# Kernel tuning notes

Hardware: AMD Instinct MI355X
Metric: run time of the kernel (lower is better)

The kernel has to match this reference:

```python
import jax, jax.numpy as jnp
import numpy as np

N, C, V, T = 256, 256, 25, 20
K = 3            # kernel_size
PAD = 1          # padding
O = 256          # out_channels
C4 = C // 4
EPS = 1e-5


def _bn(x, p, axes_shape):
    # p: (4, dim) = gamma, beta, running_mean, running_var (eval-mode BN)
    g, b, m, v = (p[i].reshape(axes_shape) for i in range(4))
    return (x - m) * (g / jnp.sqrt(v + EPS)) + b


def setup_inputs() -> dict:
    key = jax.random.key(0)
    ks = jax.random.split(key, 12)
    rn = lambda k, s, sc=0.05: jax.random.normal(k, s, jnp.float32) * sc
    bn = lambda k, d: jnp.stack([
        1.0 + 0.1 * jax.random.normal(jax.random.fold_in(k, 0), (d,), jnp.float32),  # gamma
        0.1 * jax.random.normal(jax.random.fold_in(k, 1), (d,), jnp.float32),        # beta
        0.1 * jax.random.normal(jax.random.fold_in(k, 2), (d,), jnp.float32),        # mean
        0.5 + jax.random.uniform(jax.random.fold_in(k, 3), (d,), jnp.float32),       # var
    ])
    return {
        "x": jax.random.normal(ks[0], (N, C, V, T), jnp.float32),
        "Wg1": rn(ks[1], (2 * T, T), 0.2),      # Linear T -> 2T (no bias)
        "Wg2": rn(ks[2], (K, 2 * T), 0.2),      # Linear 2T -> K (no bias)
        "Wl1": rn(ks[3], (C4, C, K)),           # Conv1d C -> C/4, kernel K
        "Wl2": rn(ks[4], (C, C4)),              # Conv1d C/4 -> C, kernel 1
        "Wc2": rn(ks[5], (O, C)),               # 1x1 Conv2d C -> O (no bias)
        "bng": bn(ks[6], 2 * T),
        "bnl": bn(ks[7], C4),
        "bn1p": bn(ks[8], C),
        "bn2p": bn(ks[9], O),
    }


def reference(x, Wg1, Wg2, Wl1, Wl2, Wc2, bng, bnl, bn1p, bn2p):
    n, c, v, t = x.shape
    new_x = jnp.transpose(x, (0, 1, 3, 2))            # (N, C, T, V)
    pooled = new_x.mean(axis=-1)                       # (N, C, T)  adaptive_avg_pool over V

    # --- G branch: per-(n,c) dynamic temporal kernel ---
    h = pooled.reshape(n * c, t) @ Wg1.T               # (NC, 2T)
    h = jax.nn.relu(_bn(h, bng, (1, 2 * t)))
    kern = jax.nn.softmax(h @ Wg2.T, axis=-1)          # (NC, K)
    kern = kern.reshape(n, c, K)

    # --- L branch: local temporal excitation ---
    l = jax.lax.conv_general_dilated(
        pooled, Wl1, window_strides=(1,), padding=[(K // 2, K // 2)],
        dimension_numbers=("NCH", "OIH", "NCH"))      # (N, C4, T)
    l = jax.nn.relu(_bn(l, bnl, (1, C4, 1)))
    l = jax.nn.sigmoid(jnp.einsum("oc,nct->not", Wl2, l))  # (N, C, T)
    new_x = new_x + l[..., None]                       # (N, C, T, V)

    # --- dynamic depthwise temporal conv (groups = N*C) ---
    padded = jnp.pad(new_x, ((0, 0), (0, 0), (PAD, PAD), (0, 0)))
    out = sum(kern[:, :, k, None, None] * padded[:, :, k:k + t, :] for k in range(K))

    out = jnp.transpose(out, (0, 1, 3, 2))             # (N, C, V, T)
    out = jax.nn.relu(_bn(out, bn1p, (1, c, 1, 1)))    # bn1 + relu; dropout in eval = identity
    out = jnp.einsum("oc,ncvt->novt", Wc2, out)        # 1x1 conv
    out = jax.nn.relu(_bn(out, bn2p, (1, O, 1, 1)))    # bn2 + relu
    return out
```

## Files before the change

kernel.cpp:

```cpp
#include <hip/hip_runtime.h>
#include <hip/hip_bf16.h>
#include <math.h>

#define N_ 256
#define C_ 256
#define V_ 25
#define T_ 20
#define C4_ 64
#define O_ 256
#define VT_ 500
#define EPS_ 1e-5f

typedef unsigned short ushort_t;
typedef unsigned short us4 __attribute__((ext_vector_type(4)));
typedef short short8 __attribute__((ext_vector_type(8)));
typedef float f32x4 __attribute__((ext_vector_type(4)));

__device__ __forceinline__ float bf2f(ushort_t u) {
    unsigned int v = ((unsigned int)u) << 16;
    return __builtin_bit_cast(float, v);
}
__device__ __forceinline__ ushort_t f2bf(float f) {
    unsigned int u = __builtin_bit_cast(unsigned int, f);
    unsigned int r = u + 0x7fffu + ((u >> 16) & 1u);
    return (ushort_t)(r >> 16);
}

__device__ __forceinline__ void bar_lds() {
    __builtin_amdgcn_sched_barrier(0);
    asm volatile("s_waitcnt lgkmcnt(0)" ::: "memory");
    __builtin_amdgcn_s_barrier();
    __builtin_amdgcn_sched_barrier(0);
}

__global__ __launch_bounds__(256) void k_pool(const float* __restrict__ x,
                                              float* __restrict__ pooled,
                                              const float* __restrict__ Wc2,
                                              ushort_t* __restrict__ wbf,
                                              const float* __restrict__ Wl1,
                                              ushort_t* __restrict__ awl,
                                              const float* __restrict__ Wl2,
                                              ushort_t* __restrict__ wl2bf) {
    int tid = threadIdx.x;
    if (blockIdx.x >= 8272) {
        int o = (blockIdx.x - 8272) * 256 + tid;
        int c4 = o / 768;
        int rem = o - c4 * 768;
        int k = rem >> 8, c = rem & 255;
        awl[o] = f2bf(Wl1[(c4 * 256 + c) * 3 + k]);
        return;
    }
    if (blockIdx.x >= 8256) {
        int i = (blockIdx.x - 8256) * 256 + tid;
        f32x4 v = ((const f32x4*)Wl2)[i];
        us4 o; o.x = f2bf(v.x); o.y = f2bf(v.y); o.z = f2bf(v.z); o.w = f2bf(v.w);
        ((us4*)wl2bf)[i] = o;
        return;
    }
    if (blockIdx.x >= 8192) {
        int i = (blockIdx.x - 8192) * 256 + tid;
        f32x4 v = ((const f32x4*)Wc2)[i];
        us4 o; o.x = f2bf(v.x); o.y = f2bf(v.y); o.z = f2bf(v.z); o.w = f2bf(v.w);
        ((us4*)wbf)[i] = o;
        return;
    }
    __shared__ float xs[8][504];
    const f32x4* src = (const f32x4*)(x + (size_t)blockIdx.x * 8 * VT_);
    for (int i = tid; i < 1000; i += 256) {
        int r = i / 125, cidx = (i % 125) * 4;
        *(f32x4*)&xs[r][cidx] = src[i];
    }
    __syncthreads();
    if (tid < 160) {
        int r = tid / 20, t = tid % 20;
        float s = 0.f;
#pragma unroll
        for (int v = 0; v < V_; ++v) s += xs[r][v * T_ + t];
        pooled[blockIdx.x * 160 + tid] = s * 0.04f;
    }
}

__global__ __launch_bounds__(256) void k_gl(const float* __restrict__ pooled,
                                            const float* __restrict__ Wg1,
                                            const float* __restrict__ Wg2,
                                            const float* __restrict__ bng,
                                            const float* __restrict__ bnl,
                                            const ushort_t* __restrict__ awl,
                                            const ushort_t* __restrict__ wl2bf,
                                            float* __restrict__ kern,
                                            float* __restrict__ l2out) {
    __shared__ __align__(16) char smem[76288];
    float (*pp)[22] = (float (*)[22])smem;
    float* sl = (float*)(smem + 22528);
    float* bl = (float*)(smem + 22528 + 256);
    char* lsT = smem + 23040;
    char* bpt = smem + 27136;

    int tid = threadIdx.x;
    int n = blockIdx.x;

    {
        const f32x4* pn = (const f32x4*)(pooled + n * (C_ * T_));
#pragma unroll
        for (int q = 0; q < 5; ++q) {
            int id = q * 256 + tid;
            int c = id / 5, qq = id % 5;
            f32x4 v = pn[id];
            pp[c][qq * 4 + 0] = v.x; pp[c][qq * 4 + 1] = v.y;
            pp[c][qq * 4 + 2] = v.z; pp[c][qq * 4 + 3] = v.w;
        }
    }
    if (tid < C4_) {
        float g = bnl[tid], b = bnl[64 + tid];
        float m = bnl[128 + tid], v = bnl[192 + tid];
        float s = g * rsqrtf(v + EPS_);
        sl[tid] = s; bl[tid] = b - m * s;
    }
    {
        unsigned int* z = (unsigned int*)lsT;
        for (int i = tid; i < 384; i += 256) z[640 + i] = 0u;
    }
    __syncthreads();

    float p[20];
#pragma unroll
    for (int t = 0; t < 20; ++t) p[t] = pp[tid][t];

    {
        float l0 = 0.f, l1 = 0.f, l2 = 0.f;
#pragma unroll 4
        for (int j = 0; j < 40; ++j) {
            float h = 0.f;
#pragma unroll
            for (int t = 0; t < 20; ++t) h = fmaf(Wg1[j * 20 + t], p[t], h);
            float g = bng[j], b = bng[40 + j];
            float m = bng[80 + j], v = bng[120 + j];
            float s = g * rsqrtf(v + EPS_);
            h = fmaxf(fmaf(h, s, b - m * s), 0.f);
            l0 = fmaf(Wg2[j], h, l0);
            l1 = fmaf(Wg2[40 + j], h, l1);
            l2 = fmaf(Wg2[80 + j], h, l2);
        }
        float mx = fmaxf(l0, fmaxf(l1, l2));
        float e0 = __expf(l0 - mx), e1 = __expf(l1 - mx), e2 = __expf(l2 - mx);
        float inv = 1.f / (e0 + e1 + e2);
        float* kp = kern + (n * C_ + tid) * 3;
        kp[0] = e0 * inv; kp[1] = e1 * inv; kp[2] = e2 * inv;
    }

    {
        int c = tid;
#pragma unroll
        for (int k = 0; k < 3; ++k) {
            int col2base = (k * 256 + c) * 2;
#pragma unroll
            for (int t = 0; t < 20; ++t) {
                int i = t + k - 1;
                float v = (i >= 0 && i < 20) ? p[i] : 0.f;
                int byte = t * 1536 + (col2base ^ ((t & 7) << 4));
                *(ushort_t*)(bpt + byte) = f2bf(v);
            }
        }
    }
    __syncthreads();

    int lane = tid & 63, wave = tid >> 6;
    int mrow = lane & 15, kof = (lane >> 4) * 8, prow = (lane >> 4) * 4;

    {
        f32x4 acc0 = (f32x4){0.f, 0.f, 0.f, 0.f};
        f32x4 acc1 = (f32x4){0.f, 0.f, 0.f, 0.f};
        int swz = ((mrow & 7) << 4);
#pragma unroll 4
        for (int kk = 0; kk < 768; kk += 32) {
            short8 af = *(const short8*)(awl + (wave * 16 + mrow) * 768 + kk + kof);
            short8 b0 = *(const short8*)(bpt + mrow * 1536 + (((kk + kof) * 2) ^ swz));
            short8 b1 = *(const short8*)(bpt + (16 + mrow) * 1536 + (((kk + kof) * 2) ^ swz));
            acc0 = __builtin_amdgcn_mfma_f32_16x16x32_bf16(af, b0, acc0, 0, 0, 0);
            acc1 = __builtin_amdgcn_mfma_f32_16x16x32_bf16(af, b1, acc1, 0, 0, 0);
        }
        f32x4 sv = *(const f32x4*)(sl + wave * 16 + prow);
        f32x4 bv = *(const f32x4*)(bl + wave * 16 + prow);
#pragma unroll
        for (int nt = 0; nt < 2; ++nt) {
            int t = nt * 16 + (lane & 15);
            if (t < 20) {
                f32x4 a = nt ? acc1 : acc0;
#pragma unroll
                for (int r = 0; r < 4; ++r) {
                    int c4 = wave * 16 + prow + r;
                    float v = fmaxf(fmaf(a[r], sv[r], bv[r]), 0.f);
                    int byte = t * 128 + ((c4 * 2) ^ ((t & 7) << 4));
                    *(ushort_t*)(lsT + byte) = f2bf(v);
                }
            }
        }
    }
    __syncthreads();

    {
        f32x4 acc[4][2];
#pragma unroll
        for (int mtl = 0; mtl < 4; ++mtl)
#pragma unroll
            for (int nt = 0; nt < 2; ++nt) acc[mtl][nt] = (f32x4){0.f, 0.f, 0.f, 0.f};
        int swz = ((mrow & 7) << 4);
#pragma unroll
        for (int kk = 0; kk < 64; kk += 32) {
            short8 af[4], bfr[2];
#pragma unroll
            for (int mtl = 0; mtl < 4; ++mtl)
                af[mtl] = *(const short8*)(wl2bf + (wave * 64 + mtl * 16 + mrow) * 64 + kk + kof);
#pragma unroll
            for (int nt = 0; nt < 2; ++nt)
                bfr[nt] = *(const short8*)(lsT + (nt * 16 + mrow) * 128 + (((kk + kof) * 2) ^ swz));
#pragma unroll
            for (int mtl = 0; mtl < 4; ++mtl)
#pragma unroll
                for (int nt = 0; nt < 2; ++nt)
                    acc[mtl][nt] = __builtin_amdgcn_mfma_f32_16x16x32_bf16(af[mtl], bfr[nt], acc[mtl][nt], 0, 0, 0);
        }
#pragma unroll
        for (int nt = 0; nt < 2; ++nt) {
            int t = nt * 16 + (lane & 15);
            if (t < 20) {
#pragma unroll
                for (int mtl = 0; mtl < 4; ++mtl) {
#pragma unroll
                    for (int r = 0; r < 4; ++r) {
                        int c = wave * 64 + mtl * 16 + prow + r;
                        float v = acc[mtl][nt][r];
                        l2out[(n * C_ + c) * T_ + t] = 1.f / (1.f + __expf(-v));
                    }
                }
            }
        }
    }
}

#define YSTRIDE 264

template <int NT>
__device__ __forceinline__ void gemm_pass(const ushort_t* __restrict__ yT,
                                          const ushort_t* __restrict__ wbf,
                                          float* __restrict__ outn,
                                          const int (&ctb)[NT], int ov_idx,
                                          int obase, int mrow, int kof, int prow,
                                          float s2, float b2) {
    f32x4 acc[4][NT];
#pragma unroll
    for (int mt = 0; mt < 4; ++mt)
#pragma unroll
        for (int j = 0; j < NT; ++j) acc[mt][j] = (f32x4){0.f, 0.f, 0.f, 0.f};

#pragma unroll 1
    for (int kk = 0; kk < C_; kk += 32) {
        short8 af[4];
        short8 bfr[NT];
#pragma unroll
        for (int mt = 0; mt < 4; ++mt)
            af[mt] = *(const short8*)(wbf + (obase + mt * 16 + mrow) * C_ + kk + kof);
#pragma unroll
        for (int j = 0; j < NT; ++j)
            bfr[j] = *(const short8*)(yT + (ctb[j] + mrow) * YSTRIDE + kk + kof);
#pragma unroll
        for (int mt = 0; mt < 4; ++mt)
#pragma unroll
            for (int j = 0; j < NT; ++j)
                acc[mt][j] = __builtin_amdgcn_mfma_f32_16x16x32_bf16(af[mt], bfr[j], acc[mt][j], 0, 0, 0);
    }

#pragma unroll
    for (int mt = 0; mt < 4; ++mt) {
#pragma unroll
        for (int r = 0; r < 4; ++r) {
            int lsrc = mt * 16 + prow + r;
            float s2w = __shfl(s2, lsrc);
            float b2w = __shfl(b2, lsrc);
            float* orow = outn + (size_t)(obase + lsrc) * VT_;
#pragma unroll
            for (int j = 0; j < NT; ++j) {
                bool skip = (j == ov_idx) && (mrow < 12);
                if (!skip) {
                    float vr = fmaxf(fmaf(acc[mt][j][r], s2w, b2w), 0.f);
                    orow[ctb[j] + mrow] = vr;
                }
            }
        }
    }
}

__global__ __launch_bounds__(256, 3) void k_main(const float* __restrict__ x,
                                                 const ushort_t* __restrict__ wbf,
                                                 const float* __restrict__ bn1p,
                                                 const float* __restrict__ bn2p,
                                                 const float* __restrict__ kern,
                                                 const float* __restrict__ l2g,
                                                 float* __restrict__ out) {
    __shared__ __align__(16) ushort_t yT[100 * YSTRIDE];

    int tid = threadIdx.x;
    int n = blockIdx.y;
    int vblk = blockIdx.x;
    const float* xn = x + (size_t)n * (C_ * V_ * T_) + vblk * 100;

    float s1, b1, k0, k1, k2, s2, b2, l2r[20];
    {
        int c = tid;
        float g1 = bn1p[c], be1 = bn1p[256 + c];
        float m1 = bn1p[512 + c], v1 = bn1p[768 + c];
        s1 = g1 * rsqrtf(v1 + EPS_);
        b1 = be1 - m1 * s1;
        float g2 = bn2p[c], be2 = bn2p[256 + c];
        float m2 = bn2p[512 + c], v2 = bn2p[768 + c];
        s2 = g2 * rsqrtf(v2 + EPS_);
        b2 = be2 - m2 * s2;
        const float* kp = kern + (n * C_ + c) * 3;
        k0 = kp[0]; k1 = kp[1]; k2 = kp[2];
        const f32x4* lp = (const f32x4*)(l2g + (n * C_ + c) * T_);
#pragma unroll
        for (int q = 0; q < 5; ++q) {
            f32x4 v = lp[q];
            l2r[q*4+0] = v.x; l2r[q*4+1] = v.y; l2r[q*4+2] = v.z; l2r[q*4+3] = v.w;
        }
    }

    int offg[5], offs[5];
#pragma unroll
    for (int q = 0; q < 5; ++q) {
        int id = q * 256 + tid;
        int c = id / 5, qq = id % 5;
        offg[q] = c * VT_ + qq * 4;
        offs[q] = c * 20 + qq * 4;
    }

    f32x4 ld[2][5];
#pragma unroll
    for (int q = 0; q < 5; ++q) ld[0][q] = *(const f32x4*)(xn + offg[q]);
#pragma unroll
    for (int q = 0; q < 5; ++q) ld[1][q] = *(const f32x4*)(xn + offg[q] + 20);

#pragma unroll
    for (int vl = 0; vl < 5; ++vl) {
        const int cur = vl & 1;
        ushort_t* xs = yT + vl * 20 * YSTRIDE;
#pragma unroll
        for (int q = 0; q < 5; ++q) {
            us4 o; o.x = f2bf(ld[cur][q].x); o.y = f2bf(ld[cur][q].y);
            o.z = f2bf(ld[cur][q].z); o.w = f2bf(ld[cur][q].w);
            *(us4*)(xs + offs[q]) = o;
        }
        if (vl < 3) {
#pragma unroll
            for (int q = 0; q < 5; ++q)
                ld[cur][q] = *(const f32x4*)(xn + offg[q] + (vl + 2) * 20);
        }
        bar_lds();
        float a[22];
        a[0] = 0.f; a[21] = 0.f;
        {
            const ushort_t* xrow = xs + tid * 20;
#pragma unroll
            for (int qq = 0; qq < 5; ++qq) {
                us4 u = *(const us4*)(xrow + qq * 4);
                a[qq*4 + 1] = bf2f(u.x) + l2r[qq*4 + 0];
                a[qq*4 + 2] = bf2f(u.y) + l2r[qq*4 + 1];
                a[qq*4 + 3] = bf2f(u.z) + l2r[qq*4 + 2];
                a[qq*4 + 4] = bf2f(u.w) + l2r[qq*4 + 3];
            }
        }
        bar_lds();
        {
            ushort_t* yrow = yT + vl * 20 * YSTRIDE + tid;
#pragma unroll
            for (int t = 0; t < 20; ++t) {
                float z = fmaf(k0, a[t], fmaf(k1, a[t + 1], k2 * a[t + 2]));
                yrow[t * YSTRIDE] = f2bf(fmaxf(fmaf(z, s1, b1), 0.f));
            }
        }
    }
    bar_lds();

    int lane = tid & 63;
    int wave = tid >> 6;
    int mrow = lane & 15;
    int kof = (lane >> 4) * 8;
    int prow = (lane >> 4) * 4;
    int obase = wave * 64;
    float* outn = out + (size_t)n * (O_ * VT_) + vblk * 100;

    {
        const int ctb0[4] = {0, 16, 32, 48};
        gemm_pass<4>(yT, wbf, outn, ctb0, -1, obase, mrow, kof, prow, s2, b2);
    }
    {
        const int ctb1[3] = {64, 80, 84};
        gemm_pass<3>(yT, wbf, outn, ctb1, 2, obase, mrow, kof, prow, s2, b2);
    }
}

extern "C" void kernel_launch(void* const* d_in, const int* in_sizes, int n_in,
                              void* d_out, int out_size, void* d_ws, size_t ws_size,
                              hipStream_t stream) {
    const float* x   = (const float*)d_in[0];
    const float* Wg1 = (const float*)d_in[1];
    const float* Wg2 = (const float*)d_in[2];
    const float* Wl1 = (const float*)d_in[3];
    const float* Wl2 = (const float*)d_in[4];
    const float* Wc2 = (const float*)d_in[5];
    const float* bng = (const float*)d_in[6];
    const float* bnl = (const float*)d_in[7];
    const float* bn1p = (const float*)d_in[8];
    const float* bn2p = (const float*)d_in[9];
    float* out = (float*)d_out;

    float* ws = (float*)d_ws;
    float* pooled = ws;
    float* kern   = ws + 1310720;
    float* l2g    = ws + 1310720 + 196608;
    ushort_t* wbf   = (ushort_t*)(ws + 2818048);
    ushort_t* wl2bf = (ushort_t*)(ws + 2818048 + 32768);
    ushort_t* awl   = (ushort_t*)(ws + 2818048 + 40960);

    k_pool<<<dim3(8464), dim3(256), 0, stream>>>(x, pooled, Wc2, wbf, Wl1, awl, Wl2, wl2bf);
    k_gl<<<dim3(N_), dim3(256), 0, stream>>>(pooled, Wg1, Wg2, bng, bnl, awl, wl2bf, kern, l2g);
    k_main<<<dim3(5, N_), dim3(256), 0, stream>>>(x, wbf, bn1p, bn2p, kern, l2g, out);
}
```

Measured before the change: 352.5 us.

## Process one batch per 512-thread block with register-resident weights and double-buffered LDS

Rewrites the main kernel so each block handles a whole batch sample. It loops over five 100-column tiles and double-buffers the LDS activation tiles. The next tile's global loads are issued before the current tile's MFMA GEMM, so memory latency overlaps with compute. The 1x1-conv weight fragments are loaded into registers once per block instead of reloaded from global every k-step of every tile. The cost is a grid of only 256 blocks, more register pressure and roughly double the LDS, which lowers occupancy and may leave latency less well hidden.

```diff
diff --git a/kernel.cpp b/kernel.cpp
--- a/kernel.cpp
+++ b/kernel.cpp
@@ -239,163 +239,241 @@
 }
 
 #define YSTRIDE 264
-
-template <int NT>
-__device__ __forceinline__ void gemm_pass(const ushort_t* __restrict__ yT,
-                                          const ushort_t* __restrict__ wbf,
-                                          float* __restrict__ outn,
-                                          const int (&ctb)[NT], int ov_idx,
-                                          int obase, int mrow, int kof, int prow,
-                                          float s2, float b2) {
-    f32x4 acc[4][NT];
-#pragma unroll
-    for (int mt = 0; mt < 4; ++mt)
-#pragma unroll
-        for (int j = 0; j < NT; ++j) acc[mt][j] = (f32x4){0.f, 0.f, 0.f, 0.f};
-
-#pragma unroll 1
-    for (int kk = 0; kk < C_; kk += 32) {
-        short8 af[4];
-        short8 bfr[NT];
-#pragma unroll
-        for (int mt = 0; mt < 4; ++mt)
-            af[mt] = *(const short8*)(wbf + (obase + mt * 16 + mrow) * C_ + kk + kof);
-#pragma unroll
-        for (int j = 0; j < NT; ++j)
-            bfr[j] = *(const short8*)(yT + (ctb[j] + mrow) * YSTRIDE + kk + kof);
-#pragma unroll
-        for (int mt = 0; mt < 4; ++mt)
-#pragma unroll
-            for (int j = 0; j < NT; ++j)
-                acc[mt][j] = __builtin_amdgcn_mfma_f32_16x16x32_bf16(af[mt], bfr[j], acc[mt][j], 0, 0, 0);
-    }
-
-#pragma unroll
-    for (int mt = 0; mt < 4; ++mt) {
-#pragma unroll
-        for (int r = 0; r < 4; ++r) {
-            int lsrc = mt * 16 + prow + r;
-            float s2w = __shfl(s2, lsrc);
-            float b2w = __shfl(b2, lsrc);
-            float* orow = outn + (size_t)(obase + lsrc) * VT_;
-#pragma unroll
-            for (int j = 0; j < NT; ++j) {
-                bool skip = (j == ov_idx) && (mrow < 12);
-                if (!skip) {
-                    float vr = fmaxf(fmaf(acc[mt][j][r], s2w, b2w), 0.f);
-                    orow[ctb[j] + mrow] = vr;
-                }
-            }
-        }
-    }
-}
-
-__global__ __launch_bounds__(256, 3) void k_main(const float* __restrict__ x,
+#define YBUF 26400
+
+__global__ __launch_bounds__(512, 2) void k_main(const float* __restrict__ x,
                                                  const ushort_t* __restrict__ wbf,
                                                  const float* __restrict__ bn1p,
                                                  const float* __restrict__ bn2p,
                                                  const float* __restrict__ kern,
                                                  const float* __restrict__ l2g,
                                                  float* __restrict__ out) {
-    __shared__ __align__(16) ushort_t yT[100 * YSTRIDE];
+    __shared__ __align__(16) ushort_t yTs[2 * YBUF];
 
     int tid = threadIdx.x;
-    int n = blockIdx.y;
-    int vblk = blockIdx.x;
-    const float* xn = x + (size_t)n * (C_ * V_ * T_) + vblk * 100;
-
-    float s1, b1, k0, k1, k2, s2, b2, l2r[20];
-    {
-        int c = tid;
-        float g1 = bn1p[c], be1 = bn1p[256 + c];
-        float m1 = bn1p[512 + c], v1 = bn1p[768 + c];
-        s1 = g1 * rsqrtf(v1 + EPS_);
-        b1 = be1 - m1 * s1;
-        float g2 = bn2p[c], be2 = bn2p[256 + c];
-        float m2 = bn2p[512 + c], v2 = bn2p[768 + c];
-        s2 = g2 * rsqrtf(v2 + EPS_);
-        b2 = be2 - m2 * s2;
-        const float* kp = kern + (n * C_ + c) * 3;
-        k0 = kp[0]; k1 = kp[1]; k2 = kp[2];
-        const f32x4* lp = (const f32x4*)(l2g + (n * C_ + c) * T_);
-#pragma unroll
-        for (int q = 0; q < 5; ++q) {
-            f32x4 v = lp[q];
-            l2r[q*4+0] = v.x; l2r[q*4+1] = v.y; l2r[q*4+2] = v.z; l2r[q*4+3] = v.w;
-        }
-    }
-
-    int offg[5], offs[5];
-#pragma unroll
-    for (int q = 0; q < 5; ++q) {
-        int id = q * 256 + tid;
-        int c = id / 5, qq = id % 5;
-        offg[q] = c * VT_ + qq * 4;
-        offs[q] = c * 20 + qq * 4;
-    }
-
-    f32x4 ld[2][5];
-#pragma unroll
-    for (int q = 0; q < 5; ++q) ld[0][q] = *(const f32x4*)(xn + offg[q]);
-#pragma unroll
-    for (int q = 0; q < 5; ++q) ld[1][q] = *(const f32x4*)(xn + offg[q] + 20);
-
-#pragma unroll
-    for (int vl = 0; vl < 5; ++vl) {
-        const int cur = vl & 1;
-        ushort_t* xs = yT + vl * 20 * YSTRIDE;
-#pragma unroll
-        for (int q = 0; q < 5; ++q) {
-            us4 o; o.x = f2bf(ld[cur][q].x); o.y = f2bf(ld[cur][q].y);
-            o.z = f2bf(ld[cur][q].z); o.w = f2bf(ld[cur][q].w);
-            *(us4*)(xs + offs[q]) = o;
-        }
-        if (vl < 3) {
-#pragma unroll
-            for (int q = 0; q < 5; ++q)
-                ld[cur][q] = *(const f32x4*)(xn + offg[q] + (vl + 2) * 20);
-        }
-        bar_lds();
-        float a[22];
-        a[0] = 0.f; a[21] = 0.f;
-        {
-            const ushort_t* xrow = xs + tid * 20;
-#pragma unroll
-            for (int qq = 0; qq < 5; ++qq) {
-                us4 u = *(const us4*)(xrow + qq * 4);
-                a[qq*4 + 1] = bf2f(u.x) + l2r[qq*4 + 0];
-                a[qq*4 + 2] = bf2f(u.y) + l2r[qq*4 + 1];
-                a[qq*4 + 3] = bf2f(u.z) + l2r[qq*4 + 2];
-                a[qq*4 + 4] = bf2f(u.w) + l2r[qq*4 + 3];
-            }
-        }
-        bar_lds();
-        {
-            ushort_t* yrow = yT + vl * 20 * YSTRIDE + tid;
-#pragma unroll
-            for (int t = 0; t < 20; ++t) {
-                float z = fmaf(k0, a[t], fmaf(k1, a[t + 1], k2 * a[t + 2]));
-                yrow[t * YSTRIDE] = f2bf(fmaxf(fmaf(z, s1, b1), 0.f));
-            }
-        }
-    }
-    bar_lds();
-
+    int n = blockIdx.x;
+    const float* xn = x + (size_t)n * (C_ * V_ * T_);
     int lane = tid & 63;
     int wave = tid >> 6;
     int mrow = lane & 15;
     int kof = (lane >> 4) * 8;
     int prow = (lane >> 4) * 4;
-    int obase = wave * 64;
-    float* outn = out + (size_t)n * (O_ * VT_) + vblk * 100;
-
-    {
-        const int ctb0[4] = {0, 16, 32, 48};
-        gemm_pass<4>(yT, wbf, outn, ctb0, -1, obase, mrow, kof, prow, s2, b2);
-    }
-    {
-        const int ctb1[3] = {64, 80, 84};
-        gemm_pass<3>(yT, wbf, outn, ctb1, 2, obase, mrow, kof, prow, s2, b2);
+    int obase = wave * 32;
+
+    float s1, b1, k0, k1, k2, l2r[20];
+    {
+        int c = tid & 255;
+        float g1 = bn1p[c], be1 = bn1p[256 + c];
+        float m1 = bn1p[512 + c], v1 = bn1p[768 + c];
+        s1 = g1 * rsqrtf(v1 + EPS_);
+        b1 = be1 - m1 * s1;
+        const float* kp = kern + (n * C_ + c) * 3;
+        k0 = kp[0]; k1 = kp[1]; k2 = kp[2];
+        const f32x4* lp = (const f32x4*)(l2g + (n * C_ + c) * T_);
+#pragma unroll
+        for (int q = 0; q < 5; ++q) {
+            f32x4 v = lp[q];
+            l2r[q*4+0] = v.x; l2r[q*4+1] = v.y; l2r[q*4+2] = v.z; l2r[q*4+3] = v.w;
+        }
+    }
+    float s2, b2;
+    {
+        int c2 = obase + (lane & 31);
+        float g2 = bn2p[c2], be2 = bn2p[256 + c2];
+        float m2 = bn2p[512 + c2], v2 = bn2p[768 + c2];
+        s2 = g2 * rsqrtf(v2 + EPS_);
+        b2 = be2 - m2 * s2;
+    }
+
+    short8 afr[2][8];
+#pragma unroll
+    for (int mt = 0; mt < 2; ++mt)
+#pragma unroll
+        for (int k8 = 0; k8 < 8; ++k8)
+            afr[mt][k8] = *(const short8*)(wbf + (obase + mt * 16 + mrow) * C_ + k8 * 32 + kof);
+
+    int off[13];
+#pragma unroll
+    for (int q = 0; q < 12; ++q) {
+        int id = q * 512 + tid;
+        off[q] = (id / 25) * VT_ + (id % 25) * 4;
+    }
+    off[12] = ((6144 + tid) / 25) * VT_ + ((6144 + tid) % 25) * 4;
+
+    const int ctb[7] = {0, 16, 32, 48, 64, 80, 84};
+
+    f32x4 ld[13];
+#pragma unroll
+    for (int q = 0; q < 12; ++q) ld[q] = *(const f32x4*)(xn + off[q]);
+    if (tid < 256) ld[12] = *(const f32x4*)(xn + off[12]);
+
+    {
+        ushort_t* xs = yTs;
+#pragma unroll
+        for (int q = 0; q < 12; ++q) {
+            int id = q * 512 + tid;
+            us4 o; o.x = f2bf(ld[q].x); o.y = f2bf(ld[q].y);
+            o.z = f2bf(ld[q].z); o.w = f2bf(ld[q].w);
+            *(us4*)(xs + (id / 25) * 100 + (id % 25) * 4) = o;
+        }
+        if (tid < 256) {
+            int id = 6144 + tid;
+            us4 o; o.x = f2bf(ld[12].x); o.y = f2bf(ld[12].y);
+            o.z = f2bf(ld[12].z); o.w = f2bf(ld[12].w);
+            *(us4*)(xs + (id / 25) * 100 + (id % 25) * 4) = o;
+        }
+    }
+    bar_lds();
+    float yv[3][20];
+    {
+        const ushort_t* xs = yTs;
+        int c = tid & 255;
+#pragma unroll
+        for (int r3 = 0; r3 < 3; ++r3) {
+            int v = (r3 < 2) ? (r3 * 2 + (tid >> 8)) : 4;
+            if (r3 < 2 || tid < 256) {
+                float a[22];
+                a[0] = 0.f; a[21] = 0.f;
+#pragma unroll
+                for (int qq = 0; qq < 5; ++qq) {
+                    us4 u = *(const us4*)(xs + c * 100 + v * 20 + qq * 4);
+                    a[qq*4 + 1] = bf2f(u.x) + l2r[qq*4 + 0];
+                    a[qq*4 + 2] = bf2f(u.y) + l2r[qq*4 + 1];
+                    a[qq*4 + 3] = bf2f(u.z) + l2r[qq*4 + 2];
+                    a[qq*4 + 4] = bf2f(u.w) + l2r[qq*4 + 3];
+                }
+#pragma unroll
+                for (int t = 0; t < 20; ++t) {
+                    float z = fmaf(k0, a[t], fmaf(k1, a[t + 1], k2 * a[t + 2]));
+                    yv[r3][t] = fmaxf(fmaf(z, s1, b1), 0.f);
+                }
+            }
+        }
+    }
+    bar_lds();
+    {
+        ushort_t* yb = yTs;
+        int c = tid & 255;
+#pragma unroll
+        for (int r3 = 0; r3 < 3; ++r3) {
+            int v = (r3 < 2) ? (r3 * 2 + (tid >> 8)) : 4;
+            if (r3 < 2 || tid < 256) {
+#pragma unroll
+                for (int t = 0; t < 20; ++t)
+                    yb[(v * 20 + t) * YSTRIDE + c] = f2bf(yv[r3][t]);
+            }
+        }
+    }
+    bar_lds();
+
+    int buf = 0;
+    float* outn0 = out + (size_t)n * (O_ * VT_);
+
+#pragma unroll 1
+    for (int tile = 0; tile < 5; ++tile) {
+        if (tile < 4) {
+#pragma unroll
+            for (int q = 0; q < 12; ++q)
+                ld[q] = *(const f32x4*)(xn + off[q] + (tile + 1) * 100);
+            if (tid < 256) ld[12] = *(const f32x4*)(xn + off[12] + (tile + 1) * 100);
+        }
+        __builtin_amdgcn_sched_barrier(0);
+
+        {
+            const ushort_t* yb = yTs + buf * YBUF;
+            f32x4 acc[2][7];
+#pragma unroll
+            for (int mt = 0; mt < 2; ++mt)
+#pragma unroll
+                for (int j = 0; j < 7; ++j) acc[mt][j] = (f32x4){0.f, 0.f, 0.f, 0.f};
+#pragma unroll
+            for (int k8 = 0; k8 < 8; ++k8) {
+#pragma unroll
+                for (int ct = 0; ct < 7; ++ct) {
+                    short8 b = *(const short8*)(yb + (ctb[ct] + mrow) * YSTRIDE + k8 * 32 + kof);
+                    acc[0][ct] = __builtin_amdgcn_mfma_f32_16x16x32_bf16(afr[0][k8], b, acc[0][ct], 0, 0, 0);
+                    acc[1][ct] = __builtin_amdgcn_mfma_f32_16x16x32_bf16(afr[1][k8], b, acc[1][ct], 0, 0, 0);
+                }
+            }
+#pragma unroll
+            for (int mt = 0; mt < 2; ++mt) {
+#pragma unroll
+                for (int r = 0; r < 4; ++r) {
+                    int lsrc = mt * 16 + prow + r;
+                    float s2w = __shfl(s2, lsrc);
+                    float b2w = __shfl(b2, lsrc);
+                    float* orow = outn0 + (size_t)(obase + lsrc) * VT_ + tile * 100;
+#pragma unroll
+                    for (int j = 0; j < 7; ++j) {
+                        if (!(j == 6 && mrow < 12)) {
+                            orow[ctb[j] + mrow] =
+                                fmaxf(fmaf(acc[mt][j][r], s2w, b2w), 0.f);
+                        }
+                    }
+                }
+            }
+        }
+
+        if (tile < 4) {
+            ushort_t* xs = yTs + (buf ^ 1) * YBUF;
+#pragma unroll
+            for (int q = 0; q < 12; ++q) {
+                int id = q * 512 + tid;
+                us4 o; o.x = f2bf(ld[q].x); o.y = f2bf(ld[q].y);
+                o.z = f2bf(ld[q].z); o.w = f2bf(ld[q].w);
+                *(us4*)(xs + (id / 25) * 100 + (id % 25) * 4) = o;
+            }
+            if (tid < 256) {
+                int id = 6144 + tid;
+                us4 o; o.x = f2bf(ld[12].x); o.y = f2bf(ld[12].y);
+                o.z = f2bf(ld[12].z); o.w = f2bf(ld[12].w);
+                *(us4*)(xs + (id / 25) * 100 + (id % 25) * 4) = o;
+            }
+        }
+        bar_lds();
+
+        if (tile < 4) {
+            const ushort_t* xs = yTs + (buf ^ 1) * YBUF;
+            int c = tid & 255;
+#pragma unroll
+            for (int r3 = 0; r3 < 3; ++r3) {
+                int v = (r3 < 2) ? (r3 * 2 + (tid >> 8)) : 4;
+                if (r3 < 2 || tid < 256) {
+                    float a[22];
+                    a[0] = 0.f; a[21] = 0.f;
+#pragma unroll
+                    for (int qq = 0; qq < 5; ++qq) {
+                        us4 u = *(const us4*)(xs + c * 100 + v * 20 + qq * 4);
+                        a[qq*4 + 1] = bf2f(u.x) + l2r[qq*4 + 0];
+                        a[qq*4 + 2] = bf2f(u.y) + l2r[qq*4 + 1];
+                        a[qq*4 + 3] = bf2f(u.z) + l2r[qq*4 + 2];
+                        a[qq*4 + 4] = bf2f(u.w) + l2r[qq*4 + 3];
+                    }
+#pragma unroll
+                    for (int t = 0; t < 20; ++t) {
+                        float z = fmaf(k0, a[t], fmaf(k1, a[t + 1], k2 * a[t + 2]));
+                        yv[r3][t] = fmaxf(fmaf(z, s1, b1), 0.f);
+                    }
+                }
+            }
+        }
+        bar_lds();
+
+        if (tile < 4) {
+            ushort_t* yb = yTs + (buf ^ 1) * YBUF;
+            int c = tid & 255;
+#pragma unroll
+            for (int r3 = 0; r3 < 3; ++r3) {
+                int v = (r3 < 2) ? (r3 * 2 + (tid >> 8)) : 4;
+                if (r3 < 2 || tid < 256) {
+#pragma unroll
+                    for (int t = 0; t < 20; ++t)
+                        yb[(v * 20 + t) * YSTRIDE + c] = f2bf(yv[r3][t]);
+                }
+            }
+        }
+        bar_lds();
+        buf ^= 1;
     }
 }
 
@@ -424,5 +502,5 @@
 
     k_pool<<<dim3(8464), dim3(256), 0, stream>>>(x, pooled, Wc2, wbf, Wl1, awl, Wl2, wl2bf);
     k_gl<<<dim3(N_), dim3(256), 0, stream>>>(pooled, Wg1, Wg2, bng, bnl, awl, wl2bf, kern, l2g);
-    k_main<<<dim3(5, N_), dim3(256), 0, stream>>>(x, wbf, bn1p, bn2p, kern, l2g, out);
-}
+    k_main<<<dim3(N_), dim3(512), 0, stream>>>(x, wbf, bn1p, bn2p, kern, l2g, out);
+}
```

After: 418.1 us. 18.6% more time.

## Load x rows directly per thread instead of staging through LDS

Applied to the files above, without the earlier changes.

Each thread now reads its own channel's 20 contiguous floats per v-block straight from global memory, replacing the coalesced cooperative load, bf16 staging in LDS and the two barriers per iteration. This removes LDS round trips, barriers and the extra bf16 rounding of x. The cost is poorly coalesced global reads, since each thread strides 500 floats apart. It also unrolls the GEMM k-loop by 2 to expose more MFMA/load overlap, at some register cost.

```diff
diff --git a/kernel.cpp b/kernel.cpp
--- a/kernel.cpp
+++ b/kernel.cpp
@@ -253,7 +253,7 @@
 #pragma unroll
         for (int j = 0; j < NT; ++j) acc[mt][j] = (f32x4){0.f, 0.f, 0.f, 0.f};
 
-#pragma unroll 1
+#pragma unroll 2
     for (int kk = 0; kk < C_; kk += 32) {
         short8 af[4];
         short8 bfr[NT];
@@ -325,58 +325,26 @@
         }
     }
 
-    int offg[5], offs[5];
-#pragma unroll
-    for (int q = 0; q < 5; ++q) {
-        int id = q * 256 + tid;
-        int c = id / 5, qq = id % 5;
-        offg[q] = c * VT_ + qq * 4;
-        offs[q] = c * 20 + qq * 4;
-    }
-
-    f32x4 ld[2][5];
-#pragma unroll
-    for (int q = 0; q < 5; ++q) ld[0][q] = *(const f32x4*)(xn + offg[q]);
-#pragma unroll
-    for (int q = 0; q < 5; ++q) ld[1][q] = *(const f32x4*)(xn + offg[q] + 20);
-
 #pragma unroll
     for (int vl = 0; vl < 5; ++vl) {
-        const int cur = vl & 1;
-        ushort_t* xs = yT + vl * 20 * YSTRIDE;
-#pragma unroll
-        for (int q = 0; q < 5; ++q) {
-            us4 o; o.x = f2bf(ld[cur][q].x); o.y = f2bf(ld[cur][q].y);
-            o.z = f2bf(ld[cur][q].z); o.w = f2bf(ld[cur][q].w);
-            *(us4*)(xs + offs[q]) = o;
-        }
-        if (vl < 3) {
-#pragma unroll
-            for (int q = 0; q < 5; ++q)
-                ld[cur][q] = *(const f32x4*)(xn + offg[q] + (vl + 2) * 20);
-        }
-        bar_lds();
+        const float* xrow = xn + tid * VT_ + vl * 20;
+        f32x4 r[5];
+#pragma unroll
+        for (int q = 0; q < 5; ++q) r[q] = *(const f32x4*)(xrow + q * 4);
         float a[22];
         a[0] = 0.f; a[21] = 0.f;
-        {
-            const ushort_t* xrow = xs + tid * 20;
-#pragma unroll
-            for (int qq = 0; qq < 5; ++qq) {
-                us4 u = *(const us4*)(xrow + qq * 4);
-                a[qq*4 + 1] = bf2f(u.x) + l2r[qq*4 + 0];
-                a[qq*4 + 2] = bf2f(u.y) + l2r[qq*4 + 1];
-                a[qq*4 + 3] = bf2f(u.z) + l2r[qq*4 + 2];
-                a[qq*4 + 4] = bf2f(u.w) + l2r[qq*4 + 3];
-            }
-        }
-        bar_lds();
-        {
-            ushort_t* yrow = yT + vl * 20 * YSTRIDE + tid;
-#pragma unroll
-            for (int t = 0; t < 20; ++t) {
-                float z = fmaf(k0, a[t], fmaf(k1, a[t + 1], k2 * a[t + 2]));
-                yrow[t * YSTRIDE] = f2bf(fmaxf(fmaf(z, s1, b1), 0.f));
-            }
+#pragma unroll
+        for (int q = 0; q < 5; ++q) {
+            a[q*4 + 1] = r[q].x + l2r[q*4 + 0];
+            a[q*4 + 2] = r[q].y + l2r[q*4 + 1];
+            a[q*4 + 3] = r[q].z + l2r[q*4 + 2];
+            a[q*4 + 4] = r[q].w + l2r[q*4 + 3];
+        }
+        ushort_t* ycol = yT + (vl * 20) * YSTRIDE + tid;
+#pragma unroll
+        for (int t = 0; t < 20; ++t) {
+            float z = fmaf(k0, a[t], fmaf(k1, a[t + 1], k2 * a[t + 2]));
+            ycol[t * YSTRIDE] = f2bf(fmaxf(fmaf(z, s1, b1), 0.f));
         }
     }
     bar_lds();
```

Measured after the change: 350.0 us. Within noise of the previous version (-0.7%).
